# Performance work log

Hardware: AMD Instinct MI355X
Metric: run time of the kernel (lower is better)

The kernel has to match this reference:

```python
import jax, jax.numpy as jnp
import numpy as np

B, S, D_IN, D_H, D_OUT, N_LAYERS = 16, 2048, 512, 1024, 10, 2


def setup_inputs() -> dict:
    key = jax.random.key(0)
    ks = jax.random.split(key, 12)
    s = lambda fan_in: 1.0 / np.sqrt(fan_in)
    return {
        "input_vec": jax.random.normal(ks[0], (B, S, D_IN), jnp.float32),
        "game_vector": jax.random.normal(ks[1], (B, N_LAYERS, D_H), jnp.float32),
        "user_vector": jax.random.normal(ks[2], (B, N_LAYERS, D_H), jnp.float32),
        # input_fc: Linear(D_IN, 2*D_IN) -> ReLU -> Linear(2*D_IN, D_H) -> ReLU
        "W1": jax.random.uniform(ks[3], (D_IN, 2 * D_IN), jnp.float32, -s(D_IN), s(D_IN)),
        "b1": jnp.zeros((2 * D_IN,), jnp.float32),
        "W2": jax.random.uniform(ks[4], (2 * D_IN, D_H), jnp.float32, -s(2 * D_IN), s(2 * D_IN)),
        "b2": jnp.zeros((D_H,), jnp.float32),
        # output_fc: Linear(D_H, D_H//2) -> ReLU -> Linear(D_H//2, D_OUT) -> LogSoftmax
        "W3": jax.random.uniform(ks[5], (D_H, D_H // 2), jnp.float32, -s(D_H), s(D_H)),
        "b3": jnp.zeros((D_H // 2,), jnp.float32),
        "W4": jax.random.uniform(ks[6], (D_H // 2, D_OUT), jnp.float32, -s(D_H // 2), s(D_H // 2)),
        "b4": jnp.zeros((D_OUT,), jnp.float32),
    }


def _causal_attention(h):
    # unscaled causal self-attention: softmax(h h^T + triu(-inf)) h
    scores = jnp.einsum("bsd,btd->bst", h, h)  # [B,S,S]
    seq = h.shape[1]
    causal = jnp.tril(jnp.ones((seq, seq), dtype=bool))
    scores = jnp.where(causal[None], scores, -jnp.inf)
    attn = jax.nn.softmax(scores, axis=-1)
    return jnp.einsum("bst,btd->bsd", attn, h)


def reference(input_vec, game_vector, user_vector, W1, b1, W2, b2, W3, b3, W4, b4):
    h = jax.nn.relu(input_vec @ W1 + b1)  # dropout is identity in eval
    h = jax.nn.relu(h @ W2 + b2)          # [B,S,D_H]
    ctx = _causal_attention(h)
    o = jax.nn.relu(ctx @ W3 + b3)
    out = jax.nn.log_softmax(o @ W4 + b4, axis=-1)
    return out, game_vector, user_vector
```

## Files before the change

kernel.cpp:

```cpp
#include <hip/hip_runtime.h>
#include <stdint.h>

#define B_   16
#define S_   2048
#define DIN  512
#define DH   1024
#define DOUT 10

typedef unsigned short u16;
typedef unsigned int   u32;

typedef __bf16 bf16_t;
typedef bf16_t bf16x8 __attribute__((ext_vector_type(8)));
typedef float  f32x4  __attribute__((ext_vector_type(4)));

#define MASKVAL (-3.0e4f)
#define PZ_U16 ((size_t)160 * 16384)

__device__ __forceinline__ float b2f(u16 u) {
    union { u32 i; float f; } v; v.i = ((u32)u) << 16; return v.f;
}
__device__ __forceinline__ u16 f2b(float f) {
    union { float f; u32 i; } v; v.f = f;
    u32 u = v.i;
    u32 r = (u + 0x7FFFu + ((u >> 16) & 1u)) >> 16;
    return (u16)r;
}
__device__ __forceinline__ u32 pack2(float a, float b) {
    return (u32)f2b(a) | ((u32)f2b(b) << 16);
}

__device__ __forceinline__ f32x4 mfma16(bf16x8 a, bf16x8 b, f32x4 c) {
    return __builtin_amdgcn_mfma_f32_16x16x32_bf16(a, b, c, 0, 0, 0);
}

__device__ __forceinline__ void load_lds16(const u16* g, u16* l) {
    __builtin_amdgcn_global_load_lds(
        (__attribute__((address_space(1))) u32*)(g),
        (__attribute__((address_space(3))) u32*)(l), 16, 0, 0);
}

template<bool F32>
__device__ __forceinline__ uint4 ld8(const void* base, size_t eidx) {
    if constexpr (F32) {
        const float* p = (const float*)base + eidx;
        float4 f0 = *(const float4*)p;
        float4 f1 = *(const float4*)(p + 4);
        uint4 r;
        r.x = pack2(f0.x, f0.y); r.y = pack2(f0.z, f0.w);
        r.z = pack2(f1.x, f1.y); r.w = pack2(f1.z, f1.w);
        return r;
    } else {
        return *(const uint4*)((const u16*)base + eidx);
    }
}

__global__ __launch_bounds__(256) void cvt_f32_bf16(
    const float* __restrict__ in, u16* __restrict__ out, int n8)
{
    int i = blockIdx.x * 256 + threadIdx.x;
    if (i >= n8) return;
    size_t e = (size_t)i * 8;
    float4 f0 = *(const float4*)(in + e);
    float4 f1 = *(const float4*)(in + e + 4);
    uint4 r;
    r.x = pack2(f0.x, f0.y); r.y = pack2(f0.z, f0.w);
    r.z = pack2(f1.x, f1.y); r.w = pack2(f1.z, f1.w);
    *(uint4*)(out + e) = r;
}

template<int QR>
__device__ __forceinline__ void rda(bf16x8 (&a)[4][2], const u16* T,
                                    int arow, int quad) {
#pragma unroll
    for (int mf = 0; mf < 4; ++mf) {
        const int row = arow + QR * 64 + mf * 16;
        const int sw = row & 7;
#pragma unroll
        for (int ks = 0; ks < 2; ++ks)
            a[mf][ks] = *(const bf16x8*)(T + row * 64 + (((ks * 4 + quad) ^ sw) << 3));
    }
}

template<int QC>
__device__ __forceinline__ void rdb(bf16x8 (&b)[2][2], const u16* T,
                                    int brow, int quad) {
#pragma unroll
    for (int nf = 0; nf < 2; ++nf) {
        const int row = brow + QC * 128 + nf * 16;
        const int sw = row & 7;
#pragma unroll
        for (int ks = 0; ks < 2; ++ks)
            b[nf][ks] = *(const bf16x8*)(T + row * 64 + (((ks * 4 + quad) ^ sw) << 3));
    }
}

template<int QR, int QC>
__device__ __forceinline__ void mmq(f32x4 (&acc)[2][2][4][2],
                                    const bf16x8 (&a)[4][2],
                                    const bf16x8 (&b)[2][2]) {
#pragma unroll
    for (int ks = 0; ks < 2; ++ks)
#pragma unroll
        for (int mf = 0; mf < 4; ++mf)
#pragma unroll
            for (int nf = 0; nf < 2; ++nf)
                acc[QR][QC][mf][nf] = mfma16(a[mf][ks], b[nf][ks], acc[QR][QC][mf][nf]);
}

#define G8BAR()  __builtin_amdgcn_s_barrier()
#define G8LGKM() do { asm volatile("s_waitcnt lgkmcnt(0)" ::: "memory"); \
                      __builtin_amdgcn_sched_barrier(0); } while (0)
#define G8VMC4() asm volatile("s_waitcnt vmcnt(4)" ::: "memory")

#define G8_LOOP_BODY(NT_)                                                     \
    const int NI = (NT_) >> 1;                                                \
    for (int i = 0; i < NI; ++i) {                                            \
        const int t1 = 2 * i + 1, t2 = 2 * i + 2, t3 = 2 * i + 3;             \
        rda<0>(a, AS_[0], arow, quad); rdb<0>(b0r, BS_[0], brow, quad);       \
        STGB(1, 2, t1); STGB(1, 3, t1);                                       \
        G8BAR(); G8LGKM();                                                    \
        __builtin_amdgcn_s_setprio(1); mmq<0, 0>(acc, a, b0r);                \
        __builtin_amdgcn_s_setprio(0); G8BAR();                               \
        rdb<1>(b1r, BS_[0], brow, quad);                                      \
        STGA(1, 1, t1); STGA(1, 3, t1);                                       \
        G8BAR(); G8LGKM();                                                    \
        __builtin_amdgcn_s_setprio(1); mmq<0, 1>(acc, a, b1r);                \
        __builtin_amdgcn_s_setprio(0); G8BAR();                               \
        rda<1>(a, AS_[0], arow, quad);                                        \
        if (t2 < (NT_)) { STGA(0, 0, t2); STGA(0, 2, t2); }                   \
        G8BAR(); G8LGKM();                                                    \
        __builtin_amdgcn_s_setprio(1); mmq<1, 0>(acc, a, b0r);                \
        __builtin_amdgcn_s_setprio(0); G8BAR();                               \
        if (t2 < (NT_)) { STGB(0, 0, t2); STGB(0, 1, t2); }                   \
        G8BAR();                                                              \
        __builtin_amdgcn_s_setprio(1); mmq<1, 1>(acc, a, b1r);                \
        __builtin_amdgcn_s_setprio(0);                                        \
        G8VMC4(); G8BAR();                                                    \
        rda<0>(a, AS_[1], arow, quad); rdb<0>(b0r, BS_[1], brow, quad);       \
        if (t2 < (NT_)) { STGB(0, 2, t2); STGB(0, 3, t2); }                   \
        G8BAR(); G8LGKM();                                                    \
        __builtin_amdgcn_s_setprio(1); mmq<0, 0>(acc, a, b0r);                \
        __builtin_amdgcn_s_setprio(0); G8BAR();                               \
        rdb<1>(b1r, BS_[1], brow, quad);                                      \
        if (t2 < (NT_)) { STGA(0, 1, t2); STGA(0, 3, t2); }                   \
        G8BAR(); G8LGKM();                                                    \
        __builtin_amdgcn_s_setprio(1); mmq<0, 1>(acc, a, b1r);                \
        __builtin_amdgcn_s_setprio(0); G8BAR();                               \
        rda<1>(a, AS_[1], arow, quad);                                        \
        if (t3 < (NT_)) { STGA(1, 0, t3); STGA(1, 2, t3); }                   \
        G8BAR(); G8LGKM();                                                    \
        __builtin_amdgcn_s_setprio(1); mmq<1, 0>(acc, a, b0r);                \
        __builtin_amdgcn_s_setprio(0); G8BAR();                               \
        if (t3 < (NT_)) { STGB(1, 0, t3); STGB(1, 1, t3); }                   \
        G8BAR();                                                              \
        __builtin_amdgcn_s_setprio(1); mmq<1, 1>(acc, a, b1r);                \
        __builtin_amdgcn_s_setprio(0);                                        \
        G8VMC4(); G8BAR();                                                    \
    }

__global__ __launch_bounds__(512, 2) void gemm8(
    const u16* __restrict__ A, const u16* __restrict__ Bt,
    const float* __restrict__ bias, u16* __restrict__ C,
    int N, int K, int do_relu)
{
    __shared__ __attribute__((aligned(16))) u16 AS_[2][16384];
    __shared__ __attribute__((aligned(16))) u16 BS_[2][16384];

    const int tid  = threadIdx.x;
    const int lane = tid & 63;
    const int w    = tid >> 6;
    const int wm   = w >> 2, wn = w & 3;
    const int quad = lane >> 4, l15 = lane & 15;
    const int m0 = blockIdx.x * 256, n0 = blockIdx.y * 256;

    const int rg = tid >> 3;
    const int ch = (lane & 7) ^ ((lane >> 3) & 7);
    const u16* gA = A  + (size_t)(m0 + rg) * K + ch * 8;
    const u16* gB = Bt + (size_t)(n0 + rg) * K + ch * 8;
    const int wslot = w * 512;

#define STGA(BUF, U, T) load_lds16(gA + (size_t)(U) * 64 * K + (T) * 64, \
                                   &AS_[BUF][(U) * 4096 + wslot])
#define STGB(BUF, U, T) load_lds16(gB + (size_t)(U) * 64 * K + (T) * 64, \
                                   &BS_[BUF][(U) * 4096 + wslot])

    f32x4 acc[2][2][4][2];
#pragma unroll
    for (int p = 0; p < 2; ++p)
#pragma unroll
    for (int q = 0; q < 2; ++q)
#pragma unroll
    for (int m = 0; m < 4; ++m)
#pragma unroll
    for (int n = 0; n < 2; ++n) acc[p][q][m][n] = (f32x4){0.f, 0.f, 0.f, 0.f};

    bf16x8 a[4][2], b0r[2][2], b1r[2][2];

    const int NT = K >> 6;

    STGA(0, 0, 0); STGA(0, 1, 0); STGA(0, 2, 0); STGA(0, 3, 0);
    STGB(0, 0, 0); STGB(0, 1, 0); STGB(0, 2, 0); STGB(0, 3, 0);
    STGA(1, 0, 1); STGA(1, 2, 1);
    STGB(1, 0, 1); STGB(1, 1, 1);
    G8VMC4(); G8BAR();

    const int arow = wm * 128 + l15;
    const int brow = wn * 32 + l15;
    G8_LOOP_BODY(NT)
#undef STGA
#undef STGB

    const int r0 = quad * 4;
#pragma unroll
    for (int qc = 0; qc < 2; ++qc)
#pragma unroll
    for (int nf = 0; nf < 2; ++nf) {
        const int col = n0 + qc * 128 + wn * 32 + nf * 16 + l15;
        const float bv = bias[col];
#pragma unroll
        for (int qr = 0; qr < 2; ++qr)
#pragma unroll
        for (int mf = 0; mf < 4; ++mf) {
            const int rowb = m0 + wm * 128 + qr * 64 + mf * 16 + r0;
#pragma unroll
            for (int r = 0; r < 4; ++r) {
                float v = acc[qr][qc][mf][nf][r] + bv;
                if (do_relu) v = fmaxf(v, 0.f);
                C[(size_t)(rowb + r) * N + col] = f2b(v);
            }
        }
    }
}

__global__ __launch_bounds__(512, 2) void score8(
    const u16* __restrict__ h, u16* __restrict__ P, int nbb)
{
    __shared__ __attribute__((aligned(16))) u16 AS_[2][16384];
    __shared__ __attribute__((aligned(16))) u16 BS_[2][16384];

    int z, t;
    if ((nbb & 7) == 0) {
        const int xcd = blockIdx.x & 7, slot = blockIdx.x >> 3;
        z = (slot / 38) * 8 + xcd;
        t = slot % 38;
    } else {
        z = blockIdx.x / 38;
        t = blockIdx.x % 38;
    }

    if (t >= 36) {
        const int p = t - 36;
        const u16 mb = f2b(MASKVAL);
        const u32 m2 = (u32)mb | ((u32)mb << 16);
        uint4 mv; mv.x = m2; mv.y = m2; mv.z = m2; mv.w = m2;
        u16* Pz0 = P + (size_t)z * PZ_U16;
#pragma unroll
        for (int i = 0; i < 8; ++i) {
            const int idx = p * 8 + i;
            const int g  = idx >> 2;
            const int mi = 4 * g + ((idx >> 1) & 1);
            const int ni = 4 * g + 2 + (idx & 1);
            u16* Pz = Pz0 + (size_t)(4 * (g + 1) * (mi - 2 * g)) * 16384;
            const size_t rstride = (size_t)(4 * (g + 1)) * 128;
            for (int q = threadIdx.x; q < 2048; q += 512) {
                int row = q >> 4, cl = (q & 15) * 8;
                *(uint4*)&Pz[(size_t)row * rstride + ni * 128 + cl] = mv;
            }
        }
        return;
    }

    int bi = 0;
    while ((bi + 1) * (bi + 2) / 2 <= t) ++bi;
    const int bj = t - bi * (bi + 1) / 2;
    const bool diag = (bi == bj);

    const int tid  = threadIdx.x;
    const int lane = tid & 63;
    const int w    = tid >> 6;
    const int wm   = w >> 2, wn = w & 3;
    const int quad = lane >> 4, l15 = lane & 15;
    const int m0 = bi * 256, n0 = bj * 256;

    const u16* hz = h + (size_t)z * S_ * DH;
    const int rg = tid >> 3;
    const int ch = (lane & 7) ^ ((lane >> 3) & 7);
    const u16* gA = hz + (size_t)(m0 + rg) * DH + ch * 8;
    const u16* gB = hz + (size_t)(n0 + rg) * DH + ch * 8;
    const int wslot = w * 512;

#define STGA(BUF, U, T) load_lds16(gA + (size_t)(U) * 64 * DH + (T) * 64, \
                                   &AS_[BUF][(U) * 4096 + wslot])
#define STGB(BUF, U, T) load_lds16(gB + (size_t)(U) * 64 * DH + (T) * 64, \
                                   &BS_[BUF][(U) * 4096 + wslot])

    f32x4 acc[2][2][4][2];
#pragma unroll
    for (int p = 0; p < 2; ++p)
#pragma unroll
    for (int q = 0; q < 2; ++q)
#pragma unroll
    for (int m = 0; m < 4; ++m)
#pragma unroll
    for (int n = 0; n < 2; ++n) acc[p][q][m][n] = (f32x4){0.f, 0.f, 0.f, 0.f};

    bf16x8 a[4][2], b0r[2][2], b1r[2][2];

    const int NT = DH >> 6;

    STGA(0, 0, 0); STGA(0, 1, 0); STGA(0, 2, 0); STGA(0, 3, 0);
    STGB(0, 0, 0); STGB(0, 1, 0); STGB(0, 2, 0); STGB(0, 3, 0);
    STGA(1, 0, 1); STGA(1, 2, 1);
    STGB(1, 0, 1); STGB(1, 1, 1);
    G8VMC4(); G8BAR();

    const int arow = wm * 128 + l15;
    const int brow = wn * 32 + l15;
    G8_LOOP_BODY(NT)
#undef STGA
#undef STGB

    const int mi = 2 * bi + wm;
    const int g  = mi >> 2;
    u16* Pz = P + (size_t)z * PZ_U16
                + (size_t)(4 * (g + 1) * (mi - 2 * g)) * 16384;
    const size_t rstride = (size_t)(4 * (g + 1)) * 128;

    const int r0 = quad * 4;
#pragma unroll
    for (int qc = 0; qc < 2; ++qc) {
        const int ni = 2 * bj + qc;
#pragma unroll
        for (int nf = 0; nf < 2; ++nf) {
            const int cl = wn * 32 + nf * 16 + l15;
            const int colg = n0 + qc * 128 + cl;
#pragma unroll
            for (int qr = 0; qr < 2; ++qr)
#pragma unroll
            for (int mf = 0; mf < 4; ++mf) {
                const int rl = qr * 64 + mf * 16 + r0;
                const int rowg = m0 + wm * 128 + rl;
#pragma unroll
                for (int r = 0; r < 4; ++r) {
                    float v = acc[qr][qc][mf][nf][r];
                    if (diag && colg > rowg + r) v = MASKVAL;
                    Pz[(size_t)(rl + r) * rstride + ni * 128 + cl] = f2b(v);
                }
            }
        }
    }
}

__global__ __launch_bounds__(512, 2) void pv8(
    const u16* __restrict__ P, const u16* __restrict__ hT,
    u16* __restrict__ ctx, int nb)
{
    __shared__ __attribute__((aligned(16))) u16 AS_[2][16384];
    __shared__ __attribute__((aligned(16))) u16 BS_[2][16384];

    const int per_bi = 4 * nb;
    const int bi  = 7 - (int)(blockIdx.x / per_bi);
    const int rem = blockIdx.x % per_bi;
    const int nj  = rem & 3;
    const int z   = rem >> 2;

    const int g  = bi >> 1;
    const int K  = (g + 1) * 512;
    const int NT = K >> 6;
    const int n0 = nj * 256;

    const u16* Az = P + (size_t)z * PZ_U16
                      + (size_t)(4 * (g + 1) * (2 * bi - 2 * g)) * 16384;
    const u16* Bz = hT + (size_t)z * DH * S_;
    u16*       C  = ctx + (size_t)z * S_ * DH;

    const int tid  = threadIdx.x;
    const int lane = tid & 63;
    const int w    = tid >> 6;
    const int wm   = w >> 2, wn = w & 3;
    const int quad = lane >> 4, l15 = lane & 15;

    const int rg = tid >> 3;
    const int ch = (lane & 7) ^ ((lane >> 3) & 7);
    const u16* gA = Az + (size_t)rg * K + ch * 8;
    const u16* gB = Bz + (size_t)(n0 + rg) * S_ + ch * 8;
    const int wslot = w * 512;

#define STGA(BUF, U, T) load_lds16(gA + (size_t)(U) * 64 * K + (T) * 64, \
                                   &AS_[BUF][(U) * 4096 + wslot])
#define STGB(BUF, U, T) load_lds16(gB + (size_t)(U) * 64 * S_ + (T) * 64, \
                                   &BS_[BUF][(U) * 4096 + wslot])

    f32x4 acc[2][2][4][2];
#pragma unroll
    for (int p = 0; p < 2; ++p)
#pragma unroll
    for (int q = 0; q < 2; ++q)
#pragma unroll
    for (int m = 0; m < 4; ++m)
#pragma unroll
    for (int n = 0; n < 2; ++n) acc[p][q][m][n] = (f32x4){0.f, 0.f, 0.f, 0.f};

    bf16x8 a[4][2], b0r[2][2], b1r[2][2];

    STGA(0, 0, 0); STGA(0, 1, 0); STGA(0, 2, 0); STGA(0, 3, 0);
    STGB(0, 0, 0); STGB(0, 1, 0); STGB(0, 2, 0); STGB(0, 3, 0);
    STGA(1, 0, 1); STGA(1, 2, 1);
    STGB(1, 0, 1); STGB(1, 1, 1);
    G8VMC4(); G8BAR();

    const int arow = wm * 128 + l15;
    const int brow = wn * 32 + l15;
    G8_LOOP_BODY(NT)
#undef STGA
#undef STGB

    const int r0 = quad * 4;
#pragma unroll
    for (int qc = 0; qc < 2; ++qc)
#pragma unroll
    for (int nf = 0; nf < 2; ++nf) {
        const int col = n0 + qc * 128 + wn * 32 + nf * 16 + l15;
#pragma unroll
        for (int qr = 0; qr < 2; ++qr)
#pragma unroll
        for (int mf = 0; mf < 4; ++mf) {
            const int rowb = bi * 256 + wm * 128 + qr * 64 + mf * 16 + r0;
#pragma unroll
            for (int r = 0; r < 4; ++r)
                C[(size_t)(rowb + r) * DH + col] = f2b(acc[qr][qc][mf][nf][r]);
        }
    }
}

__global__ __launch_bounds__(256) void score_a(
    const u16* __restrict__ h, u16* __restrict__ P)
{
    __shared__ __attribute__((aligned(16))) u16 As[128 * 32];
    __shared__ __attribute__((aligned(16))) u16 Bs[128 * 32];

    const int mi = 15 - blockIdx.x;
    const int ni = blockIdx.y;
    const int g  = mi >> 2;
    const int r4 = (g + 1) * 4;
    if (ni >= r4) return;

    const int tid = threadIdx.x;
    u16* Pz = P + (size_t)blockIdx.z * PZ_U16
                + (size_t)(4 * (g + 1) * (mi - 2 * g)) * 16384;
    const size_t rstride = (size_t)r4 * 128;

    if (ni > mi) {
        const u16 mb = f2b(MASKVAL);
        const u32 m2 = (u32)mb | ((u32)mb << 16);
        uint4 mv; mv.x = m2; mv.y = m2; mv.z = m2; mv.w = m2;
#pragma unroll
        for (int i = 0; i < 8; ++i) {
            int q = tid + i * 256;
            int row = q >> 4, cl = (q & 15) * 8;
            *(uint4*)&Pz[(size_t)row * rstride + ni * 128 + cl] = mv;
        }
        return;
    }

    const int m0 = mi * 128, n0 = ni * 128;
// ... 12 lines not shown
    u16* lA0 = &As[(w * 64) * 8];
    u16* lA1 = &As[(256 + w * 64) * 8];
    u16* lB0 = &Bs[(w * 64) * 8];
    u16* lB1 = &Bs[(256 + w * 64) * 8];

    f32x4 acc[4][4];
#pragma unroll
    for (int i = 0; i < 4; ++i)
#pragma unroll
        for (int j = 0; j < 4; ++j) acc[i][j] = (f32x4){0.f, 0.f, 0.f, 0.f};

    const int nk = DH >> 5;
    for (int kk = 0; kk < nk; ++kk) {
        load_lds16(gA0, lA0); load_lds16(gA1, lA1);
        load_lds16(gB0, lB0); load_lds16(gB1, lB1);
        gA0 += 32; gA1 += 32; gB0 += 32; gB1 += 32;
        __syncthreads();
        bf16x8 af[4], bfr[4];
#pragma unroll
        for (int i = 0; i < 4; ++i)
            af[i] = *(const bf16x8*)&As[(wm * 64 + i * 16 + l15) * 32 + quad * 8];
#pragma unroll
        for (int j = 0; j < 4; ++j)
            bfr[j] = *(const bf16x8*)&Bs[(wn * 64 + j * 16 + l15) * 32 + quad * 8];
#pragma unroll
        for (int i = 0; i < 4; ++i)
#pragma unroll
            for (int j = 0; j < 4; ++j)
                acc[i][j] = mfma16(af[i], bfr[j], acc[i][j]);
        __syncthreads();
    }

    const int r0 = quad * 4;
#pragma unroll
    for (int j = 0; j < 4; ++j) {
        int cl = wn * 64 + j * 16 + l15;
#pragma unroll
        for (int i = 0; i < 4; ++i) {
            int rl = wm * 64 + i * 16 + r0;
#pragma unroll
            for (int r = 0; r < 4; ++r) {
                int row = rl + r;
                float v = (n0 + cl <= m0 + row) ? acc[i][j][r] : MASKVAL;
                Pz[(size_t)row * rstride + ni * 128 + cl] = f2b(v);
            }
        }
    }
}

__global__ __launch_bounds__(256) void softmax_rows(u16* __restrict__ P)
{
    const int tid = threadIdx.x;
    const int lane = tid & 63, w = tid >> 6;
    const size_t row = (size_t)blockIdx.x * 4 + w;
    const int z    = (int)(row >> 11);
    const int rloc = (int)(row & (S_ - 1));
    const int mi = rloc >> 7, g = mi >> 2;
    const int kb = g + 1;
    u16* p = P + (size_t)z * PZ_U16
               + (size_t)(4 * (g + 1) * (mi - 2 * g)) * 16384
               + (size_t)(rloc & 127) * ((g + 1) * 4 * 128);
    float v[32];
    float m = -1e30f;
    for (int k = 0; k < kb; ++k) {
        uint4 u = *(const uint4*)&p[k * 512 + lane * 8];
        const u32* uu = (const u32*)&u;
#pragma unroll
        for (int i = 0; i < 4; ++i) {
            float a = b2f((u16)(uu[i] & 0xFFFFu));
            float b = b2f((u16)(uu[i] >> 16));
            v[k * 8 + 2 * i] = a; v[k * 8 + 2 * i + 1] = b;
            m = fmaxf(m, fmaxf(a, b));
        }
    }
#pragma unroll
    for (int off = 32; off >= 1; off >>= 1) m = fmaxf(m, __shfl_xor(m, off, 64));
    float s = 0.f;
    for (int k = 0; k < kb; ++k)
#pragma unroll
        for (int i = 0; i < 8; ++i) {
            float e = __expf(v[k * 8 + i] - m);
            v[k * 8 + i] = e; s += e;
        }
#pragma unroll
    for (int off = 32; off >= 1; off >>= 1) s += __shfl_xor(s, off, 64);
    float inv = 1.0f / s;
    for (int k = 0; k < kb; ++k) {
        uint4 u; u32* uu = (u32*)&u;
#pragma unroll
        for (int i = 0; i < 4; ++i)
            uu[i] = pack2(v[k * 8 + 2 * i] * inv, v[k * 8 + 2 * i + 1] * inv);
        *(uint4*)&p[k * 512 + lane * 8] = u;
    }
}

__global__ __launch_bounds__(256) void pv_a(
    const u16* __restrict__ P, const u16* __restrict__ hT, u16* __restrict__ ctx,
    int nb)
{
    __shared__ __attribute__((aligned(16))) u16 As[128 * 32];
    __shared__ __attribute__((aligned(16))) u16 Bs[128 * 32];

    const int idx = blockIdx.x;
    const int per_mi = 8 * nb;
    const int mi = 15 - (idx / per_mi);
    const int sub = idx % per_mi;
    const int nblk = sub & 7;
    const int z    = sub >> 3;
    const int g = mi >> 2;
    const int m0 = mi * 128;
    const int n0 = nblk * 128;
    const size_t rstride = (size_t)((g + 1) * 4) * 128;
    const u16* A  = P  + (size_t)z * PZ_U16
                       + (size_t)(4 * (g + 1) * (mi - 2 * g)) * 16384;
    const u16* Bt = hT + (size_t)z * DH * S_;
    u16*      C   = ctx + (size_t)z * S_ * DH;

    const int tid  = threadIdx.x;
    const int lane = tid & 63;
    const int w    = tid >> 6;
    const int wm   = w >> 1, wn = w & 1;
    const int quad = lane >> 4, l15 = lane & 15;

    const int c0 = tid, c1 = tid + 256;
    const u16* gA0 = A  + ((size_t)(c0 >> 2) * rstride + (c0 & 3) * 8);
// ... 72 lines not shown

    f32x4 acc[4][4];
#pragma unroll
    for (int i = 0; i < 4; ++i)
#pragma unroll
        for (int j = 0; j < 4; ++j) acc[i][j] = (f32x4){0.f, 0.f, 0.f, 0.f};

    uint4 va0 = ld8<AF32>(A, eA0), va1 = ld8<AF32>(A, eA1);
    uint4 vb0 = ld8<false>(Bt, eB0), vb1 = ld8<false>(Bt, eB1);

    const int nk = K >> 5;
    for (int kk = 0; kk < nk; ++kk) {
        __syncthreads();
        *(uint4*)&As[c0 * 8] = va0;
        *(uint4*)&As[c1 * 8] = va1;
        *(uint4*)&Bs[c0 * 8] = vb0;
        *(uint4*)&Bs[c1 * 8] = vb1;
        if (kk + 1 < nk) {
            eA0 += 32; eA1 += 32; eB0 += 32; eB1 += 32;
            va0 = ld8<AF32>(A, eA0); va1 = ld8<AF32>(A, eA1);
            vb0 = ld8<false>(Bt, eB0); vb1 = ld8<false>(Bt, eB1);
        }
        __syncthreads();
        bf16x8 af[4], bfr[4];
#pragma unroll
        for (int i = 0; i < 4; ++i)
            af[i] = *(const bf16x8*)&As[(wm * 64 + i * 16 + l15) * 32 + quad * 8];
#pragma unroll
        for (int j = 0; j < 4; ++j)
            bfr[j] = *(const bf16x8*)&Bs[(wn * 64 + j * 16 + l15) * 32 + quad * 8];
#pragma unroll
        for (int i = 0; i < 4; ++i)
#pragma unroll
            for (int j = 0; j < 4; ++j)
                acc[i][j] = mfma16(af[i], bfr[j], acc[i][j]);
    }

    const int r0 = quad * 4;
#pragma unroll
    for (int j = 0; j < 4; ++j) {
        int col = n0 + wn * 64 + j * 16 + l15;
        float bv = bias[col];
#pragma unroll
        for (int i = 0; i < 4; ++i) {
            int rowb = m0 + wm * 64 + i * 16 + r0;
#pragma unroll
            for (int r = 0; r < 4; ++r) {
                float v = acc[i][j][r] + bv;
                if (do_relu) v = fmaxf(v, 0.f);
                C[(size_t)(rowb + r) * N + col] = f2b(v);
            }
        }
    }
}

__global__ __launch_bounds__(256) void wprep(
    const float* __restrict__ W1, const float* __restrict__ W2,
    const float* __restrict__ W3,
    u16* __restrict__ W1t, u16* __restrict__ W2t, u16* __restrict__ W3t)
{
    __shared__ u16 t[32][33];
    int i = blockIdx.x;
    const float* in; u16* out; int R, C, xt;
    if (i < 512)       { in = W1; out = W1t; R = 512;  C = 1024; xt = 32; }
    else if (i < 1536) { in = W2; out = W2t; R = 1024; C = 1024; xt = 32; i -= 512; }
    else               { in = W3; out = W3t; R = 1024; C = 512;  xt = 16; i -= 1536; }
    const int c0 = (i % xt) * 32, r0 = (i / xt) * 32;
    const int tx = threadIdx.x, ty = threadIdx.y;
#pragma unroll
    for (int k = 0; k < 4; ++k)
        t[ty + k * 8][tx] = f2b(in[(size_t)(r0 + ty + k * 8) * C + c0 + tx]);
    __syncthreads();
#pragma unroll
    for (int k = 0; k < 4; ++k)
        out[(size_t)(c0 + ty + k * 8) * R + r0 + tx] = t[tx][ty + k * 8];
}

__global__ __launch_bounds__(256) void transpose_v(
    const u16* __restrict__ in, u16* __restrict__ out, int R, int C)
{
    __shared__ u16 st[64][33];
    const u16* ip = in  + (size_t)blockIdx.z * R * C;
    u16*       op = out + (size_t)blockIdx.z * R * C;
    const int c0 = blockIdx.x * 64, r0 = blockIdx.y * 32;
    const int t = threadIdx.x;
    {
        const int row = t >> 3, ch = t & 7;
        uint4 v = *(const uint4*)&ip[(size_t)(r0 + row) * C + c0 + ch * 8];
        const u16* pv = (const u16*)&v;
#pragma unroll
        for (int k = 0; k < 8; ++k) st[ch * 8 + k][row] = pv[k];
    }
    __syncthreads();
    {
        const int oc = t >> 2, r4 = t & 3;
        uint4 v; u16* pv = (u16*)&v;
#pragma unroll
        for (int k = 0; k < 8; ++k) pv[k] = st[oc][r4 * 8 + k];
        *(uint4*)&op[(size_t)(c0 + oc) * R + r0 + r4 * 8] = v;
    }
}

__global__ __launch_bounds__(256) void head_logsoftmax(
    const u16* __restrict__ o, const float* __restrict__ W4,
    const float* __restrict__ b4, float* __restrict__ out)
{
    __shared__ float W4s[DIN * DOUT];
    __shared__ float b4s[DOUT];
    const int tid = threadIdx.x;
    for (int i = tid; i < DIN * DOUT; i += 256) W4s[i] = W4[i];
    if (tid < DOUT) b4s[tid] = b4[tid];
    __syncthreads();
    const int lane = tid & 63, w = tid >> 6;
    for (int rr = 0; rr < 4; ++rr) {
        const size_t row = (size_t)blockIdx.x * 16 + w * 4 + rr;
        const uint4 ov = *(const uint4*)&o[row * DIN + lane * 8];
        const u32* ou = (const u32*)&ov;
        float oc[8];
#pragma unroll
        for (int i = 0; i < 4; ++i) {
            oc[2*i]   = b2f((u16)(ou[i] & 0xFFFFu));
            oc[2*i+1] = b2f((u16)(ou[i] >> 16));
        }
        float acc[DOUT];
#pragma unroll
        for (int c = 0; c < DOUT; ++c) acc[c] = 0.f;
#pragma unroll
        for (int i = 0; i < 8; ++i) {
            int k = lane * 8 + i;
            float x = oc[i];
#pragma unroll
            for (int c = 0; c < DOUT; ++c) acc[c] += x * W4s[k * DOUT + c];
        }
#pragma unroll
        for (int off = 32; off >= 1; off >>= 1)
#pragma unroll
            for (int c = 0; c < DOUT; ++c) acc[c] += __shfl_xor(acc[c], off, 64);
        float mx = -1e30f;
#pragma unroll
        for (int c = 0; c < DOUT; ++c) { acc[c] += b4s[c]; mx = fmaxf(mx, acc[c]); }
        float sum = 0.f;
#pragma unroll
        for (int c = 0; c < DOUT; ++c) sum += __expf(acc[c] - mx);
        float lse = mx + logf(sum);
        if (lane == 0) {
#pragma unroll
            for (int c = 0; c < DOUT; ++c) out[row * DOUT + c] = acc[c] - lse;
        }
    }
}

extern "C" void kernel_launch(void* const* d_in, const int* in_sizes, int n_in,
                              void* d_out, int out_size, void* d_ws, size_t ws_size,
                              hipStream_t stream) {
    const float* x  = (const float*)d_in[0];
    const float* gv = (const float*)d_in[1];
    const float* uv = (const float*)d_in[2];
    const float* W1 = (const float*)d_in[3];
    const float* b1 = (const float*)d_in[4];
    const float* W2 = (const float*)d_in[5];
    const float* b2 = (const float*)d_in[6];
    const float* W3 = (const float*)d_in[7];
    const float* b3 = (const float*)d_in[8];
    const float* W4 = (const float*)d_in[9];
    const float* b4 = (const float*)d_in[10];
    float* out = (float*)d_out;

    char* ws = (char*)d_ws;
    const size_t MB64 = (size_t)67108864;
    const size_t MiB  = (size_t)1048576;
    const size_t TIER_A3 = 2 * MB64 + 80 * MiB + 4 * MiB;
    const size_t TIER_A2 = 2 * MB64 + 72 * MiB + 8 * MiB;
    const size_t TIER_B  = 3 * MB64 + 5 * MiB;

    if (ws_size >= TIER_A3) {
        u16* h1  = (u16*)(ws);
        u16* hT  = h1;
        u16* h   = (u16*)(ws + MB64);
        u16* ctx = h;
        u16* xb  = (u16*)(ws + 2 * MB64);
        u16* P   = xb;
        u16* o   = xb;
        u16* W1t = (u16*)(ws + 2 * MB64 + 80 * MiB);
        u16* W2t = W1t + 512 * 1024;
        u16* W3t = W2t + 1024 * 1024;

        cvt_f32_bf16<<<8192, 256, 0, stream>>>(x, xb, 2097152);
        wprep<<<2048, dim3(32, 8), 0, stream>>>(W1, W2, W3, W1t, W2t, W3t);

        gemm8<<<dim3(128, 4), 512, 0, stream>>>(xb, W1t, b1, h1, 1024, 512, 1);
        gemm8<<<dim3(128, 4), 512, 0, stream>>>(h1, W2t, b2, h,  1024, 1024, 1);

        transpose_v<<<dim3(16, 64, 16), 256, 0, stream>>>(h, hT, 2048, 1024);
        score8<<<38 * 16, 512, 0, stream>>>(h, P, 16);
        softmax_rows<<<8192, 256, 0, stream>>>(P);
        pv8<<<32 * 16, 512, 0, stream>>>(P, hT, ctx, 16);

        gemm8<<<dim3(128, 2), 512, 0, stream>>>(ctx, W3t, b3, o, 512, 1024, 1);
        head_logsoftmax<<<2048, 256, 0, stream>>>(o, W4, b4, out);
    } else if (ws_size >= TIER_A2) {
        u16* h1   = (u16*)(ws);
        u16* ctx  = h1;
        u16* h    = (u16*)(ws + MB64);
        u16* o    = h;
        u16* xb   = (u16*)(ws + 2 * MB64);
        u16* hT_c = xb;
        u16* P_c  = (u16*)(ws + 2 * MB64 + 32 * MiB);
        u16* W1t  = (u16*)(ws + 2 * MB64 + 72 * MiB);
        u16* W2t  = W1t + 512 * 1024;
        u16* W3t  = W2t + 1024 * 1024;

        cvt_f32_bf16<<<8192, 256, 0, stream>>>(x, xb, 2097152);
        wprep<<<2048, dim3(32, 8), 0, stream>>>(W1, W2, W3, W1t, W2t, W3t);

        gemm8<<<dim3(128, 4), 512, 0, stream>>>(xb, W1t, b1, h1, 1024, 512, 1);
        gemm8<<<dim3(128, 4), 512, 0, stream>>>(h1, W2t, b2, h,  1024, 1024, 1);

        for (int c = 0; c < 2; ++c) {
            const u16* hc  = h   + (size_t)c * 8 * S_ * DH;
            u16*       cxc = ctx + (size_t)c * 8 * S_ * DH;
            transpose_v<<<dim3(16, 64, 8), 256, 0, stream>>>(hc, hT_c, 2048, 1024);
            score8<<<38 * 8, 512, 0, stream>>>(hc, P_c, 8);
            softmax_rows<<<4096, 256, 0, stream>>>(P_c);
            pv_a<<<16 * 8 * 8, 256, 0, stream>>>(P_c, hT_c, cxc, 8);
        }

        gemm8<<<dim3(128, 2), 512, 0, stream>>>(ctx, W3t, b3, o, 512, 1024, 1);
        head_logsoftmax<<<2048, 256, 0, stream>>>(o, W4, b4, out);
    } else if (ws_size >= TIER_B) {
        u16* h1   = (u16*)(ws);
        u16* ctx  = h1;
        u16* h    = (u16*)(ws + MB64);
        u16* xb   = (u16*)(ws + 2 * MB64);
        u16* hT_c = xb;
        u16* P_c  = (u16*)(ws + 2 * MB64 + 16 * MiB);
        u16* o    = (u16*)(ws + 2 * MB64);
        u16* W1t  = (u16*)(ws + 3 * MB64);
        u16* W2t  = W1t + 512 * 1024;
        u16* W3t  = W2t + 1024 * 1024;

        cvt_f32_bf16<<<8192, 256, 0, stream>>>(x, xb, 2097152);
        wprep<<<2048, dim3(32, 8), 0, stream>>>(W1, W2, W3, W1t, W2t, W3t);

        gemm8<<<dim3(128, 4), 512, 0, stream>>>(xb, W1t, b1, h1, 1024, 512, 1);
        gemm8<<<dim3(128, 4), 512, 0, stream>>>(h1, W2t, b2, h,  1024, 1024, 1);

        for (int c = 0; c < 4; ++c) {
            const u16* hc  = h   + (size_t)c * 4 * S_ * DH;
            u16*       cxc = ctx + (size_t)c * 4 * S_ * DH;
            transpose_v<<<dim3(16, 64, 4), 256, 0, stream>>>(hc, hT_c, 2048, 1024);
            score8<<<38 * 4, 512, 0, stream>>>(hc, P_c, 4);
            softmax_rows<<<2048, 256, 0, stream>>>(P_c);
            pv_a<<<16 * 8 * 4, 256, 0, stream>>>(P_c, hT_c, cxc, 4);
        }

        gemm8<<<dim3(128, 2), 512, 0, stream>>>(ctx, W3t, b3, o, 512, 1024, 1);
        head_logsoftmax<<<2048, 256, 0, stream>>>(o, W4, b4, out);
    } else {
        u16* h    = (u16*)(ws);
        u16* hT_b = (u16*)(ws + MB64);
        u16* P_b  = (u16*)(ws + MB64 + 4 * MiB);
        u16* ctx_b= (u16*)(ws + MB64 + 12 * MiB);
        u16* o_b  = (u16*)(ws + MB64 + 16 * MiB);
        u16* W1t  = (u16*)(ws + MB64 + 18 * MiB);
        u16* W2t  = W1t + 512 * 1024;
        u16* W3t  = W2t + 1024 * 1024;
        u16* h1_b = P_b;

        wprep<<<2048, dim3(32, 8), 0, stream>>>(W1, W2, W3, W1t, W2t, W3t);

        for (int c = 0; c < 8; ++c) {
            const float* xc = x + (size_t)c * 4096 * DIN;
            u16*         hc = h + (size_t)c * 4096 * DH;
            gemm_bt_bias_relu<true ><<<dim3(32, 8), 256, 0, stream>>>(xc, W1t, b1, h1_b,
                                                                      4096, 1024, 512, 1);
            gemm_bt_bias_relu<false><<<dim3(32, 8), 256, 0, stream>>>(h1_b, W2t, b2, hc,
                                                                      4096, 1024, 1024, 1);
        }
        for (int b = 0; b < B_; ++b) {
            const u16* hb = h + (size_t)b * S_ * DH;
            transpose_v<<<dim3(16, 64, 1), 256, 0, stream>>>(hb, hT_b, 2048, 1024);
            score_a<<<dim3(16, 16, 1), 256, 0, stream>>>(hb, P_b);
            softmax_rows<<<512, 256, 0, stream>>>(P_b);
            pv_a<<<16 * 8, 256, 0, stream>>>(P_b, hT_b, ctx_b, 1);
            gemm_bt_bias_relu<false><<<dim3(16, 4), 256, 0, stream>>>(ctx_b, W3t, b3, o_b,
                                                                      2048, 512, 1024, 1);
            head_logsoftmax<<<128, 256, 0, stream>>>(o_b, W4, b4,
                                                     out + (size_t)b * S_ * DOUT);
        }
    }

    size_t n_gv = (size_t)in_sizes[1], n_uv = (size_t)in_sizes[2];
    size_t o0 = (size_t)out_size - n_gv - n_uv;
    hipMemcpyAsync(out + o0,        gv, n_gv * 4, hipMemcpyDeviceToDevice, stream);
    hipMemcpyAsync(out + o0 + n_gv, uv, n_uv * 4, hipMemcpyDeviceToDevice, stream);
}
```

Before: 548.6 us.

## Fuse transpose into second GEMM epilogue, merge prep kernels, skip mask fill

Adds gemm8t, which writes h both row-major and transposed (staged through LDS) so the separate transpose_v pass is gone in a new large-workspace tier. It also merges the input conversion and weight transposes into one prep_all launch. Score8 no longer writes mask values into unused upper-triangle tiles; softmax_rows instead substitutes MASKVAL for out-of-range chunks. This removes a full read/write pass over h and some launches and mask stores, at the cost of a heavier GEMM epilogue and a dependence on softmax correctly ignoring the unwritten P regions.

```diff
diff --git a/kernel.cpp b/kernel.cpp
--- a/kernel.cpp
+++ b/kernel.cpp
@@ -55,18 +55,60 @@
     }
 }
 
-__global__ __launch_bounds__(256) void cvt_f32_bf16(
-    const float* __restrict__ in, u16* __restrict__ out, int n8)
-{
-    int i = blockIdx.x * 256 + threadIdx.x;
-    if (i >= n8) return;
-    size_t e = (size_t)i * 8;
-    float4 f0 = *(const float4*)(in + e);
-    float4 f1 = *(const float4*)(in + e + 4);
-    uint4 r;
-    r.x = pack2(f0.x, f0.y); r.y = pack2(f0.z, f0.w);
-    r.z = pack2(f1.x, f1.y); r.w = pack2(f1.z, f1.w);
-    *(uint4*)(out + e) = r;
+__global__ __launch_bounds__(256) void prep_all(
+    const float* __restrict__ x, u16* __restrict__ xb,
+    const float* __restrict__ W1, const float* __restrict__ W2,
+    const float* __restrict__ W3,
+    u16* __restrict__ W1t, u16* __restrict__ W2t, u16* __restrict__ W3t)
+{
+    const int tid = threadIdx.x;
+    if (blockIdx.x < 8192) {
+        size_t e = ((size_t)blockIdx.x * 256 + tid) * 8;
+        float4 f0 = *(const float4*)(x + e);
+        float4 f1 = *(const float4*)(x + e + 4);
+        uint4 r;
+        r.x = pack2(f0.x, f0.y); r.y = pack2(f0.z, f0.w);
+        r.z = pack2(f1.x, f1.y); r.w = pack2(f1.z, f1.w);
+        *(uint4*)(xb + e) = r;
+        return;
+    }
+    __shared__ u16 t[32][33];
+    int i = blockIdx.x - 8192;
+    const float* in; u16* out; int R, C, xt;
+    if (i < 512)       { in = W1; out = W1t; R = 512;  C = 1024; xt = 32; }
+    else if (i < 1536) { in = W2; out = W2t; R = 1024; C = 1024; xt = 32; i -= 512; }
+    else               { in = W3; out = W3t; R = 1024; C = 512;  xt = 16; i -= 1536; }
+    const int c0 = (i % xt) * 32, r0 = (i / xt) * 32;
+    const int tx = tid & 31, ty = tid >> 5;
+#pragma unroll
+    for (int k = 0; k < 4; ++k)
+        t[ty + k * 8][tx] = f2b(in[(size_t)(r0 + ty + k * 8) * C + c0 + tx]);
+    __syncthreads();
+#pragma unroll
+    for (int k = 0; k < 4; ++k)
+        out[(size_t)(c0 + ty + k * 8) * R + r0 + tx] = t[tx][ty + k * 8];
+}
+
+__global__ __launch_bounds__(256) void wprep(
+    const float* __restrict__ W1, const float* __restrict__ W2,
+    const float* __restrict__ W3,
+    u16* __restrict__ W1t, u16* __restrict__ W2t, u16* __restrict__ W3t)
+{
+    __shared__ u16 t[32][33];
+    int i = blockIdx.x;
+    const float* in; u16* out; int R, C, xt;
+    if (i < 512)       { in = W1; out = W1t; R = 512;  C = 1024; xt = 32; }
+    else if (i < 1536) { in = W2; out = W2t; R = 1024; C = 1024; xt = 32; i -= 512; }
+    else               { in = W3; out = W3t; R = 1024; C = 512;  xt = 16; i -= 1536; }
+    const int c0 = (i % xt) * 32, r0 = (i / xt) * 32;
+    const int tx = threadIdx.x, ty = threadIdx.y;
+#pragma unroll
+    for (int k = 0; k < 4; ++k)
+        t[ty + k * 8][tx] = f2b(in[(size_t)(r0 + ty + k * 8) * C + c0 + tx]);
+    __syncthreads();
+#pragma unroll
+    for (int k = 0; k < 4; ++k)
+        out[(size_t)(c0 + ty + k * 8) * R + r0 + tx] = t[tx][ty + k * 8];
 }
 
 template<int QR>
@@ -159,6 +201,32 @@
         G8VMC4(); G8BAR();                                                    \
     }
 
+#define G8_SETUP()                                                            \
+    const int tid  = threadIdx.x;                                             \
+    const int lane = tid & 63;                                                \
+    const int w    = tid >> 6;                                                \
+    const int wm   = w >> 2, wn = w & 3;                                      \
+    const int quad = lane >> 4, l15 = lane & 15;                              \
+    const int rg = tid >> 3;                                                  \
+    const int ch = (lane & 7) ^ ((lane >> 3) & 7);                            \
+    const int wslot = w * 512;                                                \
+    f32x4 acc[2][2][4][2];                                                    \
+    _Pragma("unroll") for (int p_ = 0; p_ < 2; ++p_)                          \
+    _Pragma("unroll") for (int q_ = 0; q_ < 2; ++q_)                          \
+    _Pragma("unroll") for (int m_ = 0; m_ < 4; ++m_)                          \
+    _Pragma("unroll") for (int n_ = 0; n_ < 2; ++n_)                          \
+        acc[p_][q_][m_][n_] = (f32x4){0.f, 0.f, 0.f, 0.f};                    \
+    bf16x8 a[4][2], b0r[2][2], b1r[2][2];                                     \
+    const int arow = wm * 128 + l15;                                          \
+    const int brow = wn * 32 + l15;
+
+#define G8_PROLOGUE()                                                         \
+    STGA(0, 0, 0); STGA(0, 1, 0); STGA(0, 2, 0); STGA(0, 3, 0);               \
+    STGB(0, 0, 0); STGB(0, 1, 0); STGB(0, 2, 0); STGB(0, 3, 0);               \
+    STGA(1, 0, 1); STGA(1, 2, 1);                                             \
+    STGB(1, 0, 1); STGB(1, 1, 1);                                             \
+    G8VMC4(); G8BAR();
+
 __global__ __launch_bounds__(512, 2) void gemm8(
     const u16* __restrict__ A, const u16* __restrict__ Bt,
     const float* __restrict__ bias, u16* __restrict__ C,
@@ -167,46 +235,18 @@
     __shared__ __attribute__((aligned(16))) u16 AS_[2][16384];
     __shared__ __attribute__((aligned(16))) u16 BS_[2][16384];
 
-    const int tid  = threadIdx.x;
-    const int lane = tid & 63;
-    const int w    = tid >> 6;
-    const int wm   = w >> 2, wn = w & 3;
-    const int quad = lane >> 4, l15 = lane & 15;
+    G8_SETUP()
     const int m0 = blockIdx.x * 256, n0 = blockIdx.y * 256;
-
-    const int rg = tid >> 3;
-    const int ch = (lane & 7) ^ ((lane >> 3) & 7);
     const u16* gA = A  + (size_t)(m0 + rg) * K + ch * 8;
     const u16* gB = Bt + (size_t)(n0 + rg) * K + ch * 8;
-    const int wslot = w * 512;
 
 #define STGA(BUF, U, T) load_lds16(gA + (size_t)(U) * 64 * K + (T) * 64, \
                                    &AS_[BUF][(U) * 4096 + wslot])
 #define STGB(BUF, U, T) load_lds16(gB + (size_t)(U) * 64 * K + (T) * 64, \
                                    &BS_[BUF][(U) * 4096 + wslot])
 
-    f32x4 acc[2][2][4][2];
-#pragma unroll
-    for (int p = 0; p < 2; ++p)
-#pragma unroll
-    for (int q = 0; q < 2; ++q)
-#pragma unroll
-    for (int m = 0; m < 4; ++m)
-#pragma unroll
-    for (int n = 0; n < 2; ++n) acc[p][q][m][n] = (f32x4){0.f, 0.f, 0.f, 0.f};
-
-    bf16x8 a[4][2], b0r[2][2], b1r[2][2];
-
     const int NT = K >> 6;
-
-    STGA(0, 0, 0); STGA(0, 1, 0); STGA(0, 2, 0); STGA(0, 3, 0);
-    STGB(0, 0, 0); STGB(0, 1, 0); STGB(0, 2, 0); STGB(0, 3, 0);
-    STGA(1, 0, 1); STGA(1, 2, 1);
-    STGB(1, 0, 1); STGB(1, 1, 1);
-    G8VMC4(); G8BAR();
-
-    const int arow = wm * 128 + l15;
-    const int brow = wn * 32 + l15;
+    G8_PROLOGUE()
     G8_LOOP_BODY(NT)
 #undef STGA
 #undef STGB
@@ -233,6 +273,80 @@
     }
 }
 
+__global__ __launch_bounds__(512, 2) void gemm8t(
+    const u16* __restrict__ A, const u16* __restrict__ Bt,
+    const float* __restrict__ bias, u16* __restrict__ C,
+    u16* __restrict__ CT, int N, int K)
+{
+    __shared__ __attribute__((aligned(16))) u16 SM[65536];
+    u16* const AS_[2] = {SM, SM + 16384};
+    u16* const BS_[2] = {SM + 32768, SM + 49152};
+
+    G8_SETUP()
+    const int m0 = blockIdx.x * 256, n0 = blockIdx.y * 256;
+    const u16* gA = A  + (size_t)(m0 + rg) * K + ch * 8;
+    const u16* gB = Bt + (size_t)(n0 + rg) * K + ch * 8;
+
+#define STGA(BUF, U, T) load_lds16(gA + (size_t)(U) * 64 * K + (T) * 64, \
+                                   &AS_[BUF][(U) * 4096 + wslot])
+#define STGB(BUF, U, T) load_lds16(gB + (size_t)(U) * 64 * K + (T) * 64, \
+                                   &BS_[BUF][(U) * 4096 + wslot])
+
+    const int NT = K >> 6;
+    G8_PROLOGUE()
+    G8_LOOP_BODY(NT)
+#undef STGA
+#undef STGB
+
+    asm volatile("s_waitcnt vmcnt(0)" ::: "memory");
+    G8BAR();
+
+    const int r0 = quad * 4;
+#pragma unroll
+    for (int qc = 0; qc < 2; ++qc)
+#pragma unroll
+    for (int nf = 0; nf < 2; ++nf) {
+        const int cl  = qc * 128 + wn * 32 + nf * 16 + l15;
+        const int col = n0 + cl;
+        const float bv = bias[col];
+#pragma unroll
+        for (int qr = 0; qr < 2; ++qr)
+#pragma unroll
+        for (int mf = 0; mf < 4; ++mf) {
+            const int rl   = wm * 128 + qr * 64 + mf * 16 + r0;
+            const int rowb = m0 + rl;
+            u16 b0 = f2b(fmaxf(acc[qr][qc][mf][nf][0] + bv, 0.f));
+            u16 b1 = f2b(fmaxf(acc[qr][qc][mf][nf][1] + bv, 0.f));
+            u16 b2 = f2b(fmaxf(acc[qr][qc][mf][nf][2] + bv, 0.f));
+            u16 b3 = f2b(fmaxf(acc[qr][qc][mf][nf][3] + bv, 0.f));
+            C[(size_t)(rowb + 0) * N + col] = b0;
+            C[(size_t)(rowb + 1) * N + col] = b1;
+            C[(size_t)(rowb + 2) * N + col] = b2;
+            C[(size_t)(rowb + 3) * N + col] = b3;
+            const int rc  = rl >> 3;
+            const int off = cl * 256 + ((rc ^ (cl & 31)) << 3) + (rl & 7);
+            uint2 wv; wv.x = (u32)b0 | ((u32)b1 << 16);
+            wv.y = (u32)b2 | ((u32)b3 << 16);
+            *(uint2*)&SM[off] = wv;
+        }
+    }
+    __syncthreads();
+
+    const int z  = m0 >> 11;
+    const int rz = m0 & 2047;
+    u16* CTz = CT + (size_t)z * DH * S_;
+    const int oc   = tid >> 1;
+    const int half = tid & 1;
+#pragma unroll
+    for (int it = 0; it < 16; ++it) {
+        const int r   = half * 128 + it * 8;
+        const int rc  = r >> 3;
+        const int off = oc * 256 + ((rc ^ (oc & 31)) << 3);
+        uint4 v = *(const uint4*)&SM[off];
+        *(uint4*)&CTz[(size_t)(n0 + oc) * S_ + rz + r] = v;
+    }
+}
+
 __global__ __launch_bounds__(512, 2) void score8(
     const u16* __restrict__ h, u16* __restrict__ P, int nbb)
 {
@@ -242,33 +356,11 @@
     int z, t;
     if ((nbb & 7) == 0) {
         const int xcd = blockIdx.x & 7, slot = blockIdx.x >> 3;
-        z = (slot / 38) * 8 + xcd;
-        t = slot % 38;
+        z = (slot / 36) * 8 + xcd;
+        t = slot % 36;
     } else {
-        z = blockIdx.x / 38;
-        t = blockIdx.x % 38;
-    }
-
-    if (t >= 36) {
-        const int p = t - 36;
-        const u16 mb = f2b(MASKVAL);
-        const u32 m2 = (u32)mb | ((u32)mb << 16);
-        uint4 mv; mv.x = m2; mv.y = m2; mv.z = m2; mv.w = m2;
-        u16* Pz0 = P + (size_t)z * PZ_U16;
-#pragma unroll
-        for (int i = 0; i < 8; ++i) {
-            const int idx = p * 8 + i;
-            const int g  = idx >> 2;
-            const int mi = 4 * g + ((idx >> 1) & 1);
-            const int ni = 4 * g + 2 + (idx & 1);
-            u16* Pz = Pz0 + (size_t)(4 * (g + 1) * (mi - 2 * g)) * 16384;
-            const size_t rstride = (size_t)(4 * (g + 1)) * 128;
-            for (int q = threadIdx.x; q < 2048; q += 512) {
-                int row = q >> 4, cl = (q & 15) * 8;
-                *(uint4*)&Pz[(size_t)row * rstride + ni * 128 + cl] = mv;
-            }
-        }
-        return;
+        z = blockIdx.x / 36;
+        t = blockIdx.x % 36;
     }
 
     int bi = 0;
@@ -276,47 +368,19 @@
     const int bj = t - bi * (bi + 1) / 2;
     const bool diag = (bi == bj);
 
-    const int tid  = threadIdx.x;
-    const int lane = tid & 63;
-    const int w    = tid >> 6;
-    const int wm   = w >> 2, wn = w & 3;
-    const int quad = lane >> 4, l15 = lane & 15;
+    G8_SETUP()
     const int m0 = bi * 256, n0 = bj * 256;
-
     const u16* hz = h + (size_t)z * S_ * DH;
-    const int rg = tid >> 3;
-    const int ch = (lane & 7) ^ ((lane >> 3) & 7);
     const u16* gA = hz + (size_t)(m0 + rg) * DH + ch * 8;
     const u16* gB = hz + (size_t)(n0 + rg) * DH + ch * 8;
-    const int wslot = w * 512;
 
 #define STGA(BUF, U, T) load_lds16(gA + (size_t)(U) * 64 * DH + (T) * 64, \
                                    &AS_[BUF][(U) * 4096 + wslot])
 #define STGB(BUF, U, T) load_lds16(gB + (size_t)(U) * 64 * DH + (T) * 64, \
                                    &BS_[BUF][(U) * 4096 + wslot])
 
-    f32x4 acc[2][2][4][2];
-#pragma unroll
-    for (int p = 0; p < 2; ++p)
-#pragma unroll
-    for (int q = 0; q < 2; ++q)
-#pragma unroll
-    for (int m = 0; m < 4; ++m)
-#pragma unroll
-    for (int n = 0; n < 2; ++n) acc[p][q][m][n] = (f32x4){0.f, 0.f, 0.f, 0.f};
-
-    bf16x8 a[4][2], b0r[2][2], b1r[2][2];
-
     const int NT = DH >> 6;
-
-    STGA(0, 0, 0); STGA(0, 1, 0); STGA(0, 2, 0); STGA(0, 3, 0);
-    STGB(0, 0, 0); STGB(0, 1, 0); STGB(0, 2, 0); STGB(0, 3, 0);
-    STGA(1, 0, 1); STGA(1, 2, 1);
-    STGB(1, 0, 1); STGB(1, 1, 1);
-    G8VMC4(); G8BAR();
-
-    const int arow = wm * 128 + l15;
-    const int brow = wn * 32 + l15;
+    G8_PROLOGUE()
     G8_LOOP_BODY(NT)
 #undef STGA
 #undef STGB
@@ -375,43 +439,16 @@
     const u16* Bz = hT + (size_t)z * DH * S_;
     u16*       C  = ctx + (size_t)z * S_ * DH;
 
-    const int tid  = threadIdx.x;
-    const int lane = tid & 63;
-    const int w    = tid >> 6;
-    const int wm   = w >> 2, wn = w & 3;
-    const int quad = lane >> 4, l15 = lane & 15;
-
-    const int rg = tid >> 3;
-    const int ch = (lane & 7) ^ ((lane >> 3) & 7);
+    G8_SETUP()
     const u16* gA = Az + (size_t)rg * K + ch * 8;
     const u16* gB = Bz + (size_t)(n0 + rg) * S_ + ch * 8;
-    const int wslot = w * 512;
 
 #define STGA(BUF, U, T) load_lds16(gA + (size_t)(U) * 64 * K + (T) * 64, \
                                    &AS_[BUF][(U) * 4096 + wslot])
 #define STGB(BUF, U, T) load_lds16(gB + (size_t)(U) * 64 * S_ + (T) * 64, \
                                    &BS_[BUF][(U) * 4096 + wslot])
 
-    f32x4 acc[2][2][4][2];
-#pragma unroll
-    for (int p = 0; p < 2; ++p)
-#pragma unroll
-    for (int q = 0; q < 2; ++q)
-#pragma unroll
-    for (int m = 0; m < 4; ++m)
-#pragma unroll
-    for (int n = 0; n < 2; ++n) acc[p][q][m][n] = (f32x4){0.f, 0.f, 0.f, 0.f};
-
-    bf16x8 a[4][2], b0r[2][2], b1r[2][2];
-
-    STGA(0, 0, 0); STGA(0, 1, 0); STGA(0, 2, 0); STGA(0, 3, 0);
-    STGB(0, 0, 0); STGB(0, 1, 0); STGB(0, 2, 0); STGB(0, 3, 0);
-    STGA(1, 0, 1); STGA(1, 2, 1);
-    STGB(1, 0, 1); STGB(1, 1, 1);
-    G8VMC4(); G8BAR();
-
-    const int arow = wm * 128 + l15;
-    const int brow = wn * 32 + l15;
+    G8_PROLOGUE()
     G8_LOOP_BODY(NT)
 #undef STGA
 #undef STGB
@@ -530,6 +567,7 @@
 {
     const int tid = threadIdx.x;
     const int lane = tid & 63, w = tid >> 6;
+    const int quad = lane >> 4;
     const size_t row = (size_t)blockIdx.x * 4 + w;
     const int z    = (int)(row >> 11);
     const int rloc = (int)(row & (S_ - 1));
@@ -541,14 +579,19 @@
     float v[32];
     float m = -1e30f;
     for (int k = 0; k < kb; ++k) {
-        uint4 u = *(const uint4*)&p[k * 512 + lane * 8];
-        const u32* uu = (const u32*)&u;
-#pragma unroll
-        for (int i = 0; i < 4; ++i) {
-            float a = b2f((u16)(uu[i] & 0xFFFFu));
-            float b = b2f((u16)(uu[i] >> 16));
-            v[k * 8 + 2 * i] = a; v[k * 8 + 2 * i + 1] = b;
-            m = fmaxf(m, fmaxf(a, b));
+        if (k * 4 + quad <= mi) {
+            uint4 u = *(const uint4*)&p[k * 512 + lane * 8];
+            const u32* uu = (const u32*)&u;
+#pragma unroll
+            for (int i = 0; i < 4; ++i) {
+                float a = b2f((u16)(uu[i] & 0xFFFFu));
+                float b = b2f((u16)(uu[i] >> 16));
+                v[k * 8 + 2 * i] = a; v[k * 8 + 2 * i + 1] = b;
+                m = fmaxf(m, fmaxf(a, b));
+            }
+        } else {
+#pragma unroll
+            for (int i = 0; i < 8; ++i) v[k * 8 + i] = MASKVAL;
         }
     }
 #pragma unroll
@@ -727,28 +770,6 @@
             }
         }
     }
-}
-
-__global__ __launch_bounds__(256) void wprep(
-    const float* __restrict__ W1, const float* __restrict__ W2,
-    const float* __restrict__ W3,
-    u16* __restrict__ W1t, u16* __restrict__ W2t, u16* __restrict__ W3t)
-{
-    __shared__ u16 t[32][33];
-    int i = blockIdx.x;
-    const float* in; u16* out; int R, C, xt;
-    if (i < 512)       { in = W1; out = W1t; R = 512;  C = 1024; xt = 32; }
-    else if (i < 1536) { in = W2; out = W2t; R = 1024; C = 1024; xt = 32; i -= 512; }
-    else               { in = W3; out = W3t; R = 1024; C = 512;  xt = 16; i -= 1536; }
-    const int c0 = (i % xt) * 32, r0 = (i / xt) * 32;
-    const int tx = threadIdx.x, ty = threadIdx.y;
-#pragma unroll
-    for (int k = 0; k < 4; ++k)
-        t[ty + k * 8][tx] = f2b(in[(size_t)(r0 + ty + k * 8) * C + c0 + tx]);
-    __syncthreads();
-#pragma unroll
-    for (int k = 0; k < 4; ++k)
-        out[(size_t)(c0 + ty + k * 8) * R + r0 + tx] = t[tx][ty + k * 8];
 }
 
 __global__ __launch_bounds__(256) void transpose_v(
@@ -844,11 +865,34 @@
     char* ws = (char*)d_ws;
     const size_t MB64 = (size_t)67108864;
     const size_t MiB  = (size_t)1048576;
+    const size_t TIER_A4 = 276 * MiB;
     const size_t TIER_A3 = 2 * MB64 + 80 * MiB + 4 * MiB;
     const size_t TIER_A2 = 2 * MB64 + 72 * MiB + 8 * MiB;
     const size_t TIER_B  = 3 * MB64 + 5 * MiB;
 
-    if (ws_size >= TIER_A3) {
+    if (ws_size >= TIER_A4) {
+        u16* h1  = (u16*)(ws);
+        u16* o   = (u16*)(ws);
+        u16* h   = (u16*)(ws + MB64);
+        u16* ctx = h;
+        u16* hT  = (u16*)(ws + 128 * MiB);
+        u16* P   = (u16*)(ws + 192 * MiB);
+        u16* xb  = hT;
+        u16* W1t = (u16*)(ws + 272 * MiB);
+        u16* W2t = W1t + 512 * 1024;
+        u16* W3t = W2t + 1024 * 1024;
+
+        prep_all<<<10240, 256, 0, stream>>>(x, xb, W1, W2, W3, W1t, W2t, W3t);
+        gemm8<<<dim3(128, 4), 512, 0, stream>>>(xb, W1t, b1, h1, 1024, 512, 1);
+        gemm8t<<<dim3(128, 4), 512, 0, stream>>>(h1, W2t, b2, h, hT, 1024, 1024);
+
+        score8<<<36 * 16, 512, 0, stream>>>(h, P, 16);
+        softmax_rows<<<8192, 256, 0, stream>>>(P);
+        pv8<<<32 * 16, 512, 0, stream>>>(P, hT, ctx, 16);
+
+        gemm8<<<dim3(128, 2), 512, 0, stream>>>(ctx, W3t, b3, o, 512, 1024, 1);
+        head_logsoftmax<<<2048, 256, 0, stream>>>(o, W4, b4, out);
+    } else if (ws_size >= TIER_A3) {
         u16* h1  = (u16*)(ws);
         u16* hT  = h1;
         u16* h   = (u16*)(ws + MB64);
@@ -860,14 +904,12 @@
         u16* W2t = W1t + 512 * 1024;
         u16* W3t = W2t + 1024 * 1024;
 
-        cvt_f32_bf16<<<8192, 256, 0, stream>>>(x, xb, 2097152);
-        wprep<<<2048, dim3(32, 8), 0, stream>>>(W1, W2, W3, W1t, W2t, W3t);
-
+        prep_all<<<10240, 256, 0, stream>>>(x, xb, W1, W2, W3, W1t, W2t, W3t);
         gemm8<<<dim3(128, 4), 512, 0, stream>>>(xb, W1t, b1, h1, 1024, 512, 1);
         gemm8<<<dim3(128, 4), 512, 0, stream>>>(h1, W2t, b2, h,  1024, 1024, 1);
 
         transpose_v<<<dim3(16, 64, 16), 256, 0, stream>>>(h, hT, 2048, 1024);
-        score8<<<38 * 16, 512, 0, stream>>>(h, P, 16);
+        score8<<<36 * 16, 512, 0, stream>>>(h, P, 16);
         softmax_rows<<<8192, 256, 0, stream>>>(P);
         pv8<<<32 * 16, 512, 0, stream>>>(P, hT, ctx, 16);
 
@@ -885,9 +927,7 @@
         u16* W2t  = W1t + 512 * 1024;
         u16* W3t  = W2t + 1024 * 1024;
 
-        cvt_f32_bf16<<<8192, 256, 0, stream>>>(x, xb, 2097152);
-        wprep<<<2048, dim3(32, 8), 0, stream>>>(W1, W2, W3, W1t, W2t, W3t);
-
+        prep_all<<<10240, 256, 0, stream>>>(x, xb, W1, W2, W3, W1t, W2t, W3t);
         gemm8<<<dim3(128, 4), 512, 0, stream>>>(xb, W1t, b1, h1, 1024, 512, 1);
         gemm8<<<dim3(128, 4), 512, 0, stream>>>(h1, W2t, b2, h,  1024, 1024, 1);
 
@@ -895,7 +935,7 @@
             const u16* hc  = h   + (size_t)c * 8 * S_ * DH;
             u16*       cxc = ctx + (size_t)c * 8 * S_ * DH;
             transpose_v<<<dim3(16, 64, 8), 256, 0, stream>>>(hc, hT_c, 2048, 1024);
-            score8<<<38 * 8, 512, 0, stream>>>(hc, P_c, 8);
+            score8<<<36 * 8, 512, 0, stream>>>(hc, P_c, 8);
             softmax_rows<<<4096, 256, 0, stream>>>(P_c);
             pv_a<<<16 * 8 * 8, 256, 0, stream>>>(P_c, hT_c, cxc, 8);
         }
@@ -914,9 +954,7 @@
         u16* W2t  = W1t + 512 * 1024;
         u16* W3t  = W2t + 1024 * 1024;
 
-        cvt_f32_bf16<<<8192, 256, 0, stream>>>(x, xb, 2097152);
-        wprep<<<2048, dim3(32, 8), 0, stream>>>(W1, W2, W3, W1t, W2t, W3t);
-
+        prep_all<<<10240, 256, 0, stream>>>(x, xb, W1, W2, W3, W1t, W2t, W3t);
         gemm8<<<dim3(128, 4), 512, 0, stream>>>(xb, W1t, b1, h1, 1024, 512, 1);
         gemm8<<<dim3(128, 4), 512, 0, stream>>>(h1, W2t, b2, h,  1024, 1024, 1);
 
@@ -924,7 +962,7 @@
             const u16* hc  = h   + (size_t)c * 4 * S_ * DH;
             u16*       cxc = ctx + (size_t)c * 4 * S_ * DH;
             transpose_v<<<dim3(16, 64, 4), 256, 0, stream>>>(hc, hT_c, 2048, 1024);
-            score8<<<38 * 4, 512, 0, stream>>>(hc, P_c, 4);
+            score8<<<36 * 4, 512, 0, stream>>>(hc, P_c, 4);
             softmax_rows<<<2048, 256, 0, stream>>>(P_c);
             pv_a<<<16 * 8 * 4, 256, 0, stream>>>(P_c, hT_c, cxc, 4);
         }
```

New measurement: 543.8 us. No clear change (-0.9%).
